# Kernel optimization log

Measured on AMD Instinct MI355X. Metric: run time of the kernel, lower is better.

## Reference

```python
import jax, jax.numpy as jnp
import numpy as np


def setup_inputs() -> dict:
    key = jax.random.key(0)
    k1, k2, k3 = jax.random.split(key, 3)
    B, T1, T2, D, MP = 16, 256, 256, 256, 32
    reps_lt = jax.random.normal(k1, (B, T1, D), dtype=jnp.float32)
    reps_rt = jax.random.normal(k2, (B, T2, D), dtype=jnp.float32)
    # keras 'uniform' initializer ~ U(-0.05, 0.05); stored as [mp, d]
    kernel = jax.random.uniform(k3, (MP, D), dtype=jnp.float32, minval=-0.05, maxval=0.05)
    return {"reps_lt": reps_lt, "reps_rt": reps_rt, "kernel": kernel}


def reference(reps_lt, reps_rt, kernel):
    # reps_lt: [b, t1, d], reps_rt: [b, t2, d], kernel: [mp, d]
    # Original: broadcast lt*kernel -> [b,t1,1,mp,d], rt -> [b,1,t2,1,d],
    # cosine_norm=False => tanh(sum over d), then max over t1.
    lt_m = reps_lt[:, :, None, :] * kernel[None, None, :, :]      # [b, t1, mp, d]
    scores = jnp.einsum('bimd,bjd->bijm', lt_m, reps_rt)           # [b, t1, t2, mp]
    match = jnp.tanh(scores)
    return jnp.max(match, axis=1)                                  # [b, t2, mp]
```

## Files before the change

### kernel.cpp

```cpp
#include <hip/hip_runtime.h>
#include <hip/hip_bf16.h>
#include <math.h>

#define Bn   16
#define T1n  256
#define T2n  256
#define Dn   256
#define MPn  32

typedef __attribute__((ext_vector_type(8))) short short8;
typedef __attribute__((ext_vector_type(4))) float f32x4;

typedef const __attribute__((address_space(1))) void* gp_t;
typedef __attribute__((address_space(3))) void* lp_t;

__device__ __forceinline__ void gl_lds16(const void* g, void* l) {
  __builtin_amdgcn_global_load_lds((gp_t)g, (lp_t)l, 16, 0, 0);
}

__device__ inline short f2b(float f) {
  __hip_bfloat16 h = __float2bfloat16(f);
  return __builtin_bit_cast(short, h);
}
__device__ inline float b2f(short s) {
  unsigned int u = ((unsigned int)(unsigned short)s) << 16;
  return __builtin_bit_cast(float, u);
}
__device__ inline float max4(f32x4 a) {
  return fmaxf(fmaxf(a.x, a.y), fmaxf(a.z, a.w));
}

__device__ inline int swz_chunk(int row, int d8) {
  return row * 32 + (d8 ^ (row & 7));
}

__global__ __launch_bounds__(256, 8)
void cvt_bf16_kernel(const float* __restrict__ lt, const float* __restrict__ rt,
                     short* __restrict__ olt, short* __restrict__ ort) {
  int blk = blockIdx.x;
  const float* src;
  short* dst;
  int t;
  if (blk < 512) { src = lt; dst = olt; t = blk * 256 + threadIdx.x; }
  else           { src = rt; dst = ort; t = (blk - 512) * 256 + threadIdx.x; }
  const f32x4* s = reinterpret_cast<const f32x4*>(src + (size_t)t * 8);
  f32x4 f0 = s[0], f1 = s[1];
  short8 v;
  v[0] = f2b(f0.x); v[1] = f2b(f0.y); v[2] = f2b(f0.z); v[3] = f2b(f0.w);
  v[4] = f2b(f1.x); v[5] = f2b(f1.y); v[6] = f2b(f1.z); v[7] = f2b(f1.w);
  *reinterpret_cast<short8*>(dst + (size_t)t * 8) = v;
}

__global__ __launch_bounds__(256, 3)
void mp_match_kernel(const short* __restrict__ ltb,
                     const short* __restrict__ rtb,
                     const float* __restrict__ kern,
                     float* __restrict__ out) {
  __shared__ short lds_rt[32 * 256];
  __shared__ short lds_lt[2][32 * 256];

  const int bid = blockIdx.x;
  const int xcd = bid & 7;
  const int idx = bid >> 3;
  const int b   = ((idx >> 6) << 3) | xcd;
  const int rem = idx & 63;
  const int jblk = rem & 7;
  const int mg   = rem >> 3;
  const int j0   = jblk * 32;

  const int tid  = threadIdx.x;
  const int lane = tid & 63;
  const int w    = tid >> 6;
  const int m    = mg * 4 + w;
  const int bl   = lane & 15;
  const int hl   = lane >> 4;

  int soff[4];
  #pragma unroll
  for (int it = 0; it < 4; ++it) {
    int cidx = it * 256 + tid;
    int row = cidx >> 5, slot = cidx & 31;
    soff[it] = row * 256 + (slot ^ (row & 7)) * 8;
  }
  const int wub = (tid & ~63) * 8;

  const short* rbase = rtb + ((size_t)b * T2n + j0) * Dn;
  #pragma unroll
  for (int it = 0; it < 4; ++it)
    gl_lds16(rbase + soff[it], &lds_rt[it * 256 * 8 + wub]);
  asm volatile("s_waitcnt vmcnt(0)" ::: "memory");
  __syncthreads();

  const short* lbase = ltb + (size_t)b * T1n * Dn;
  #pragma unroll
  for (int it = 0; it < 4; ++it)
    gl_lds16(lbase + soff[it], &lds_lt[0][it * 256 * 8 + wub]);

  short8 bsc[2][8];
  {
    const float* kbase = kern + (size_t)m * Dn;
    #pragma unroll
    for (int kk = 0; kk < 8; ++kk) {
      int d8 = kk * 4 + hl;
      const f32x4* kp = reinterpret_cast<const f32x4*>(kbase + d8 * 8);
      f32x4 k0 = kp[0], k1 = kp[1];
      #pragma unroll
      for (int sub = 0; sub < 2; ++sub) {
        int brow = sub * 16 + bl;
        short8 r = *reinterpret_cast<const short8*>(&lds_rt[swz_chunk(brow, d8) * 8]);
        short8 v;
        v[0] = f2b(b2f(r[0]) * k0.x); v[1] = f2b(b2f(r[1]) * k0.y);
        v[2] = f2b(b2f(r[2]) * k0.z); v[3] = f2b(b2f(r[3]) * k0.w);
        v[4] = f2b(b2f(r[4]) * k1.x); v[5] = f2b(b2f(r[5]) * k1.y);
        v[6] = f2b(b2f(r[6]) * k1.z); v[7] = f2b(b2f(r[7]) * k1.w);
        bsc[sub][kk] = v;
      }
    }
  }

  float jmax0 = -1e30f, jmax1 = -1e30f;

  asm volatile("s_waitcnt vmcnt(0)" ::: "memory");
  __syncthreads();

  for (int ic = 0; ic < 8; ++ic) {
    const int cur = ic & 1;
    if (ic < 7) {
      #pragma unroll
      for (int it = 0; it < 4; ++it)
        gl_lds16(lbase + (ic + 1) * 32 * 256 + soff[it],
                 &lds_lt[cur ^ 1][it * 256 * 8 + wub]);
    }
    const short* lcur = lds_lt[cur];
    f32x4 a00 = {0.f,0.f,0.f,0.f}, a01 = {0.f,0.f,0.f,0.f};
    f32x4 a10 = {0.f,0.f,0.f,0.f}, a11 = {0.f,0.f,0.f,0.f};
    #pragma unroll
    for (int kk = 0; kk < 8; ++kk) {
      int d8 = kk * 4 + hl;
      short8 A0 = *reinterpret_cast<const short8*>(&lcur[swz_chunk(bl, d8) * 8]);
      short8 A1 = *reinterpret_cast<const short8*>(&lcur[swz_chunk(16 + bl, d8) * 8]);
      a00 = __builtin_amdgcn_mfma_f32_16x16x32_bf16(A0, bsc[0][kk], a00, 0, 0, 0);
      a01 = __builtin_amdgcn_mfma_f32_16x16x32_bf16(A0, bsc[1][kk], a01, 0, 0, 0);
      a10 = __builtin_amdgcn_mfma_f32_16x16x32_bf16(A1, bsc[0][kk], a10, 0, 0, 0);
      a11 = __builtin_amdgcn_mfma_f32_16x16x32_bf16(A1, bsc[1][kk], a11, 0, 0, 0);
    }
    jmax0 = fmaxf(jmax0, fmaxf(max4(a00), max4(a10)));
    jmax1 = fmaxf(jmax1, fmaxf(max4(a01), max4(a11)));
    if (ic < 7) {
      asm volatile("s_waitcnt vmcnt(0)" ::: "memory");
      __syncthreads();
    }
  }

  jmax0 = fmaxf(jmax0, __shfl_xor(jmax0, 16));
  jmax0 = fmaxf(jmax0, __shfl_xor(jmax0, 32));
  jmax1 = fmaxf(jmax1, __shfl_xor(jmax1, 16));
  jmax1 = fmaxf(jmax1, __shfl_xor(jmax1, 32));
  if (hl < 2) {
    float v = hl ? jmax1 : jmax0;
    int j = j0 + hl * 16 + bl;
    out[((size_t)b * T2n + j) * MPn + m] = tanhf(v);
  }
}

extern "C" void kernel_launch(void* const* d_in, const int* in_sizes, int n_in,
                              void* d_out, int out_size, void* d_ws, size_t ws_size,
                              hipStream_t stream) {
  const float* lt   = (const float*)d_in[0];
  const float* rt   = (const float*)d_in[1];
  const float* kern = (const float*)d_in[2];
  float* out = (float*)d_out;

  short* ltb = (short*)d_ws;
  short* rtb = ltb + (size_t)Bn * T1n * Dn;

  cvt_bf16_kernel<<<1024, 256, 0, stream>>>(lt, rt, ltb, rtb);
  mp_match_kernel<<<1024, 256, 0, stream>>>(ltb, rtb, kern, out);
}
```

Before: 28.68 us.

## Drop LDS staging and read bf16 operands directly from global memory

Removes the shared-memory double buffer and async global-to-LDS copies. Each wave now loads its MFMA A and B fragments straight from global memory, relying on L2/L1 caching since the four waves of a block read the same lt rows. The inner loop becomes 16 chunks of 16 rows with two MFMAs per step, and occupancy is raised to 4 blocks per SIMD. This removes block-wide barriers and LDS traffic, but exposes global load latency with no explicit prefetch and makes each wave issue redundant global loads.

```diff
diff --git a/kernel.cpp b/kernel.cpp
--- a/kernel.cpp
+++ b/kernel.cpp
@@ -11,13 +11,6 @@
 typedef __attribute__((ext_vector_type(8))) short short8;
 typedef __attribute__((ext_vector_type(4))) float f32x4;
 
-typedef const __attribute__((address_space(1))) void* gp_t;
-typedef __attribute__((address_space(3))) void* lp_t;
-
-__device__ __forceinline__ void gl_lds16(const void* g, void* l) {
-  __builtin_amdgcn_global_load_lds((gp_t)g, (lp_t)l, 16, 0, 0);
-}
-
 __device__ inline short f2b(float f) {
   __hip_bfloat16 h = __float2bfloat16(f);
   return __builtin_bit_cast(short, h);
@@ -28,10 +21,6 @@
 }
 __device__ inline float max4(f32x4 a) {
   return fmaxf(fmaxf(a.x, a.y), fmaxf(a.z, a.w));
-}
-
-__device__ inline int swz_chunk(int row, int d8) {
-  return row * 32 + (d8 ^ (row & 7));
 }
 
 __global__ __launch_bounds__(256, 8)
@@ -51,14 +40,11 @@
   *reinterpret_cast<short8*>(dst + (size_t)t * 8) = v;
 }
 
-__global__ __launch_bounds__(256, 3)
+__global__ __launch_bounds__(256, 4)
 void mp_match_kernel(const short* __restrict__ ltb,
                      const short* __restrict__ rtb,
                      const float* __restrict__ kern,
                      float* __restrict__ out) {
-  __shared__ short lds_rt[32 * 256];
-  __shared__ short lds_lt[2][32 * 256];
-
   const int bid = blockIdx.x;
   const int xcd = bid & 7;
   const int idx = bid >> 3;
@@ -75,81 +61,44 @@
   const int bl   = lane & 15;
   const int hl   = lane >> 4;
 
-  int soff[4];
-  #pragma unroll
-  for (int it = 0; it < 4; ++it) {
-    int cidx = it * 256 + tid;
-    int row = cidx >> 5, slot = cidx & 31;
-    soff[it] = row * 256 + (slot ^ (row & 7)) * 8;
-  }
-  const int wub = (tid & ~63) * 8;
+  const short* ltbase = ltb + (size_t)b * T1n * Dn;
+  const short* rtbase = rtb + ((size_t)b * T2n + j0) * Dn;
+  const float* kbase  = kern + (size_t)m * Dn;
 
-  const short* rbase = rtb + ((size_t)b * T2n + j0) * Dn;
-  #pragma unroll
-  for (int it = 0; it < 4; ++it)
-    gl_lds16(rbase + soff[it], &lds_rt[it * 256 * 8 + wub]);
-  asm volatile("s_waitcnt vmcnt(0)" ::: "memory");
-  __syncthreads();
-
-  const short* lbase = ltb + (size_t)b * T1n * Dn;
-  #pragma unroll
-  for (int it = 0; it < 4; ++it)
-    gl_lds16(lbase + soff[it], &lds_lt[0][it * 256 * 8 + wub]);
+  const int foff = bl * Dn + hl * 8;
 
   short8 bsc[2][8];
-  {
-    const float* kbase = kern + (size_t)m * Dn;
+  #pragma unroll
+  for (int kk = 0; kk < 8; ++kk) {
+    const f32x4* kp = reinterpret_cast<const f32x4*>(kbase + (kk * 4 + hl) * 8);
+    f32x4 k0 = kp[0], k1 = kp[1];
     #pragma unroll
-    for (int kk = 0; kk < 8; ++kk) {
-      int d8 = kk * 4 + hl;
-      const f32x4* kp = reinterpret_cast<const f32x4*>(kbase + d8 * 8);
-      f32x4 k0 = kp[0], k1 = kp[1];
-      #pragma unroll
-      for (int sub = 0; sub < 2; ++sub) {
-        int brow = sub * 16 + bl;
-        short8 r = *reinterpret_cast<const short8*>(&lds_rt[swz_chunk(brow, d8) * 8]);
-        short8 v;
-        v[0] = f2b(b2f(r[0]) * k0.x); v[1] = f2b(b2f(r[1]) * k0.y);
-        v[2] = f2b(b2f(r[2]) * k0.z); v[3] = f2b(b2f(r[3]) * k0.w);
-        v[4] = f2b(b2f(r[4]) * k1.x); v[5] = f2b(b2f(r[5]) * k1.y);
-        v[6] = f2b(b2f(r[6]) * k1.z); v[7] = f2b(b2f(r[7]) * k1.w);
-        bsc[sub][kk] = v;
-      }
+    for (int sub = 0; sub < 2; ++sub) {
+      short8 r = *reinterpret_cast<const short8*>(rtbase + sub * 16 * Dn + foff + kk * 32);
+      short8 v;
+      v[0] = f2b(b2f(r[0]) * k0.x); v[1] = f2b(b2f(r[1]) * k0.y);
+      v[2] = f2b(b2f(r[2]) * k0.z); v[3] = f2b(b2f(r[3]) * k0.w);
+      v[4] = f2b(b2f(r[4]) * k1.x); v[5] = f2b(b2f(r[5]) * k1.y);
+      v[6] = f2b(b2f(r[6]) * k1.z); v[7] = f2b(b2f(r[7]) * k1.w);
+      bsc[sub][kk] = v;
     }
   }
 
   float jmax0 = -1e30f, jmax1 = -1e30f;
 
-  asm volatile("s_waitcnt vmcnt(0)" ::: "memory");
-  __syncthreads();
-
-  for (int ic = 0; ic < 8; ++ic) {
-    const int cur = ic & 1;
-    if (ic < 7) {
-      #pragma unroll
-      for (int it = 0; it < 4; ++it)
-        gl_lds16(lbase + (ic + 1) * 32 * 256 + soff[it],
-                 &lds_lt[cur ^ 1][it * 256 * 8 + wub]);
-    }
-    const short* lcur = lds_lt[cur];
-    f32x4 a00 = {0.f,0.f,0.f,0.f}, a01 = {0.f,0.f,0.f,0.f};
-    f32x4 a10 = {0.f,0.f,0.f,0.f}, a11 = {0.f,0.f,0.f,0.f};
+  #pragma unroll 1
+  for (int ic = 0; ic < 16; ++ic) {
+    const short* abase = ltbase + ic * 16 * Dn + foff;
+    f32x4 a0 = {0.f, 0.f, 0.f, 0.f};
+    f32x4 a1 = {0.f, 0.f, 0.f, 0.f};
     #pragma unroll
     for (int kk = 0; kk < 8; ++kk) {
-      int d8 = kk * 4 + hl;
-      short8 A0 = *reinterpret_cast<const short8*>(&lcur[swz_chunk(bl, d8) * 8]);
-      short8 A1 = *reinterpret_cast<const short8*>(&lcur[swz_chunk(16 + bl, d8) * 8]);
-      a00 = __builtin_amdgcn_mfma_f32_16x16x32_bf16(A0, bsc[0][kk], a00, 0, 0, 0);
-      a01 = __builtin_amdgcn_mfma_f32_16x16x32_bf16(A0, bsc[1][kk], a01, 0, 0, 0);
-      a10 = __builtin_amdgcn_mfma_f32_16x16x32_bf16(A1, bsc[0][kk], a10, 0, 0, 0);
-      a11 = __builtin_amdgcn_mfma_f32_16x16x32_bf16(A1, bsc[1][kk], a11, 0, 0, 0);
+      short8 A = *reinterpret_cast<const short8*>(abase + kk * 32);
+      a0 = __builtin_amdgcn_mfma_f32_16x16x32_bf16(A, bsc[0][kk], a0, 0, 0, 0);
+      a1 = __builtin_amdgcn_mfma_f32_16x16x32_bf16(A, bsc[1][kk], a1, 0, 0, 0);
     }
-    jmax0 = fmaxf(jmax0, fmaxf(max4(a00), max4(a10)));
-    jmax1 = fmaxf(jmax1, fmaxf(max4(a01), max4(a11)));
-    if (ic < 7) {
-      asm volatile("s_waitcnt vmcnt(0)" ::: "memory");
-      __syncthreads();
-    }
+    jmax0 = fmaxf(jmax0, max4(a0));
+    jmax1 = fmaxf(jmax1, max4(a1));
   }
 
   jmax0 = fmaxf(jmax0, __shfl_xor(jmax0, 16));
```

Result: slower. 75.98 us (+164.9%).

## Widen j tile to 64 rows, prefetch two lt stages, halve grid

Applied to the files above, without the earlier changes.

Each block now covers 64 rt rows instead of 32, so every lt tile loaded from LDS feeds four MFMA column blocks. This halves the grid and the total lt global traffic. The lt pipeline is restructured to issue the first two stages up front, refill the just-consumed buffer after a barrier, and use partial vmcnt waits. It also raises wave priority around the MFMA loop. The cost is more registers (bsc grows to 4x8 short8) and lower occupancy (launch bounds 2), and only 512 blocks run on 256 CUs.

```diff
diff --git a/kernel.cpp b/kernel.cpp
--- a/kernel.cpp
+++ b/kernel.cpp
@@ -17,6 +17,13 @@
 __device__ __forceinline__ void gl_lds16(const void* g, void* l) {
   __builtin_amdgcn_global_load_lds((gp_t)g, (lp_t)l, 16, 0, 0);
 }
+__device__ __forceinline__ void fence() { asm volatile("" ::: "memory"); }
+__device__ __forceinline__ void bar() {
+  fence();
+  __builtin_amdgcn_s_barrier();
+  fence();
+}
+#define WAIT_VM(N) asm volatile("s_waitcnt vmcnt(" #N ")" ::: "memory")
 
 __device__ inline short f2b(float f) {
   __hip_bfloat16 h = __float2bfloat16(f);
@@ -51,22 +58,22 @@
   *reinterpret_cast<short8*>(dst + (size_t)t * 8) = v;
 }
 
-__global__ __launch_bounds__(256, 3)
+__global__ __launch_bounds__(256, 2)
 void mp_match_kernel(const short* __restrict__ ltb,
                      const short* __restrict__ rtb,
                      const float* __restrict__ kern,
                      float* __restrict__ out) {
-  __shared__ short lds_rt[32 * 256];
+  __shared__ short lds_rt[64 * 256];
   __shared__ short lds_lt[2][32 * 256];
 
   const int bid = blockIdx.x;
   const int xcd = bid & 7;
   const int idx = bid >> 3;
-  const int b   = ((idx >> 6) << 3) | xcd;
-  const int rem = idx & 63;
-  const int jblk = rem & 7;
-  const int mg   = rem >> 3;
-  const int j0   = jblk * 32;
+  const int b   = ((idx >> 5) << 3) | xcd;
+  const int rem = idx & 31;
+  const int jblk = rem & 3;
+  const int mg   = rem >> 2;
+  const int j0   = jblk * 64;
 
   const int tid  = threadIdx.x;
   const int lane = tid & 63;
@@ -75,80 +82,107 @@
   const int bl   = lane & 15;
   const int hl   = lane >> 4;
 
-  int soff[4];
+  const short* lbase = ltb + (size_t)b * T1n * Dn;
+  const short* rbase = rtb + ((size_t)b * T2n + j0) * Dn;
+  const float* kbase = kern + (size_t)m * Dn;
+
+  int soffL[4];
   #pragma unroll
   for (int it = 0; it < 4; ++it) {
     int cidx = it * 256 + tid;
     int row = cidx >> 5, slot = cidx & 31;
-    soff[it] = row * 256 + (slot ^ (row & 7)) * 8;
+    soffL[it] = row * 256 + (slot ^ (row & 7)) * 8;
   }
   const int wub = (tid & ~63) * 8;
 
-  const short* rbase = rtb + ((size_t)b * T2n + j0) * Dn;
+  f32x4 kq[8][2];
+  #pragma unroll
+  for (int kk = 0; kk < 8; ++kk) {
+    const f32x4* kp = reinterpret_cast<const f32x4*>(kbase + (kk * 4 + hl) * 8);
+    kq[kk][0] = kp[0];
+    kq[kk][1] = kp[1];
+  }
+  fence();
+  #pragma unroll
+  for (int it = 0; it < 8; ++it) {
+    int cidx = it * 256 + tid;
+    int row = cidx >> 5, slot = cidx & 31;
+    gl_lds16(rbase + row * 256 + (slot ^ (row & 7)) * 8,
+             &lds_rt[it * 256 * 8 + wub]);
+  }
+  fence();
   #pragma unroll
   for (int it = 0; it < 4; ++it)
-    gl_lds16(rbase + soff[it], &lds_rt[it * 256 * 8 + wub]);
-  asm volatile("s_waitcnt vmcnt(0)" ::: "memory");
-  __syncthreads();
-
-  const short* lbase = ltb + (size_t)b * T1n * Dn;
+    gl_lds16(lbase + soffL[it], &lds_lt[0][it * 256 * 8 + wub]);
+  fence();
   #pragma unroll
   for (int it = 0; it < 4; ++it)
-    gl_lds16(lbase + soff[it], &lds_lt[0][it * 256 * 8 + wub]);
-
-  short8 bsc[2][8];
-  {
-    const float* kbase = kern + (size_t)m * Dn;
+    gl_lds16(lbase + 32 * 256 + soffL[it], &lds_lt[1][it * 256 * 8 + wub]);
+  fence();
+
+  WAIT_VM(8);
+  bar();
+
+  short8 bsc[4][8];
+  #pragma unroll
+  for (int kk = 0; kk < 8; ++kk) {
+    f32x4 k0 = kq[kk][0], k1 = kq[kk][1];
     #pragma unroll
-    for (int kk = 0; kk < 8; ++kk) {
-      int d8 = kk * 4 + hl;
-      const f32x4* kp = reinterpret_cast<const f32x4*>(kbase + d8 * 8);
-      f32x4 k0 = kp[0], k1 = kp[1];
-      #pragma unroll
-      for (int sub = 0; sub < 2; ++sub) {
-        int brow = sub * 16 + bl;
-        short8 r = *reinterpret_cast<const short8*>(&lds_rt[swz_chunk(brow, d8) * 8]);
-        short8 v;
-        v[0] = f2b(b2f(r[0]) * k0.x); v[1] = f2b(b2f(r[1]) * k0.y);
-        v[2] = f2b(b2f(r[2]) * k0.z); v[3] = f2b(b2f(r[3]) * k0.w);
-        v[4] = f2b(b2f(r[4]) * k1.x); v[5] = f2b(b2f(r[5]) * k1.y);
-        v[6] = f2b(b2f(r[6]) * k1.z); v[7] = f2b(b2f(r[7]) * k1.w);
-        bsc[sub][kk] = v;
-      }
+    for (int sub = 0; sub < 4; ++sub) {
+      int brow = sub * 16 + bl;
+      short8 r = *reinterpret_cast<const short8*>(
+          &lds_rt[swz_chunk(brow, kk * 4 + hl) * 8]);
+      short8 v;
+      v[0] = f2b(b2f(r[0]) * k0.x); v[1] = f2b(b2f(r[1]) * k0.y);
+      v[2] = f2b(b2f(r[2]) * k0.z); v[3] = f2b(b2f(r[3]) * k0.w);
+      v[4] = f2b(b2f(r[4]) * k1.x); v[5] = f2b(b2f(r[5]) * k1.y);
+      v[6] = f2b(b2f(r[6]) * k1.z); v[7] = f2b(b2f(r[7]) * k1.w);
+      bsc[sub][kk] = v;
     }
   }
 
-  float jmax0 = -1e30f, jmax1 = -1e30f;
-
-  asm volatile("s_waitcnt vmcnt(0)" ::: "memory");
-  __syncthreads();
-
+  WAIT_VM(4);
+  bar();
+
+  float jmax0 = -1e30f, jmax1 = -1e30f, jmax2 = -1e30f, jmax3 = -1e30f;
+
+  #pragma unroll 1
   for (int ic = 0; ic < 8; ++ic) {
     const int cur = ic & 1;
-    if (ic < 7) {
+    const short* lcur = lds_lt[cur];
+    __builtin_amdgcn_s_setprio(1);
+    #pragma unroll
+    for (int it2 = 0; it2 < 2; ++it2) {
+      int arow = it2 * 16 + bl;
+      f32x4 a0 = {0.f,0.f,0.f,0.f}, a1 = {0.f,0.f,0.f,0.f};
+      f32x4 a2 = {0.f,0.f,0.f,0.f}, a3 = {0.f,0.f,0.f,0.f};
+      #pragma unroll
+      for (int kk = 0; kk < 8; ++kk) {
+        short8 A = *reinterpret_cast<const short8*>(
+            &lcur[swz_chunk(arow, kk * 4 + hl) * 8]);
+        a0 = __builtin_amdgcn_mfma_f32_16x16x32_bf16(A, bsc[0][kk], a0, 0, 0, 0);
+        a1 = __builtin_amdgcn_mfma_f32_16x16x32_bf16(A, bsc[1][kk], a1, 0, 0, 0);
+        a2 = __builtin_amdgcn_mfma_f32_16x16x32_bf16(A, bsc[2][kk], a2, 0, 0, 0);
+        a3 = __builtin_amdgcn_mfma_f32_16x16x32_bf16(A, bsc[3][kk], a3, 0, 0, 0);
+      }
+      jmax0 = fmaxf(jmax0, max4(a0));
+      jmax1 = fmaxf(jmax1, max4(a1));
+      jmax2 = fmaxf(jmax2, max4(a2));
+      jmax3 = fmaxf(jmax3, max4(a3));
+    }
+    __builtin_amdgcn_s_setprio(0);
+    bar();
+    if (ic < 6) {
       #pragma unroll
       for (int it = 0; it < 4; ++it)
-        gl_lds16(lbase + (ic + 1) * 32 * 256 + soff[it],
-                 &lds_lt[cur ^ 1][it * 256 * 8 + wub]);
-    }
-    const short* lcur = lds_lt[cur];
-    f32x4 a00 = {0.f,0.f,0.f,0.f}, a01 = {0.f,0.f,0.f,0.f};
-    f32x4 a10 = {0.f,0.f,0.f,0.f}, a11 = {0.f,0.f,0.f,0.f};
-    #pragma unroll
-    for (int kk = 0; kk < 8; ++kk) {
-      int d8 = kk * 4 + hl;
-      short8 A0 = *reinterpret_cast<const short8*>(&lcur[swz_chunk(bl, d8) * 8]);
-      short8 A1 = *reinterpret_cast<const short8*>(&lcur[swz_chunk(16 + bl, d8) * 8]);
-      a00 = __builtin_amdgcn_mfma_f32_16x16x32_bf16(A0, bsc[0][kk], a00, 0, 0, 0);
-      a01 = __builtin_amdgcn_mfma_f32_16x16x32_bf16(A0, bsc[1][kk], a01, 0, 0, 0);
-      a10 = __builtin_amdgcn_mfma_f32_16x16x32_bf16(A1, bsc[0][kk], a10, 0, 0, 0);
-      a11 = __builtin_amdgcn_mfma_f32_16x16x32_bf16(A1, bsc[1][kk], a11, 0, 0, 0);
-    }
-    jmax0 = fmaxf(jmax0, fmaxf(max4(a00), max4(a10)));
-    jmax1 = fmaxf(jmax1, fmaxf(max4(a01), max4(a11)));
-    if (ic < 7) {
-      asm volatile("s_waitcnt vmcnt(0)" ::: "memory");
-      __syncthreads();
+        gl_lds16(lbase + (ic + 2) * 32 * 256 + soffL[it],
+                 &lds_lt[cur][it * 256 * 8 + wub]);
+      fence();
+      WAIT_VM(4);
+      bar();
+    } else if (ic == 6) {
+      WAIT_VM(0);
+      bar();
     }
   }
 
@@ -156,11 +190,13 @@
   jmax0 = fmaxf(jmax0, __shfl_xor(jmax0, 32));
   jmax1 = fmaxf(jmax1, __shfl_xor(jmax1, 16));
   jmax1 = fmaxf(jmax1, __shfl_xor(jmax1, 32));
-  if (hl < 2) {
-    float v = hl ? jmax1 : jmax0;
-    int j = j0 + hl * 16 + bl;
-    out[((size_t)b * T2n + j) * MPn + m] = tanhf(v);
-  }
+  jmax2 = fmaxf(jmax2, __shfl_xor(jmax2, 16));
+  jmax2 = fmaxf(jmax2, __shfl_xor(jmax2, 32));
+  jmax3 = fmaxf(jmax3, __shfl_xor(jmax3, 16));
+  jmax3 = fmaxf(jmax3, __shfl_xor(jmax3, 32));
+  float v = (hl == 0) ? jmax0 : (hl == 1) ? jmax1 : (hl == 2) ? jmax2 : jmax3;
+  int j = j0 + hl * 16 + bl;
+  out[((size_t)b * T2n + j) * MPn + m] = tanhf(v);
 }
 
 extern "C" void kernel_launch(void* const* d_in, const int* in_sizes, int n_in,
@@ -175,5 +211,5 @@
   short* rtb = ltb + (size_t)Bn * T1n * Dn;
 
   cvt_bf16_kernel<<<1024, 256, 0, stream>>>(lt, rt, ltb, rtb);
-  mp_match_kernel<<<1024, 256, 0, stream>>>(ltb, rtb, kern, out);
-}
+  mp_match_kernel<<<512, 256, 0, stream>>>(ltb, rtb, kern, out);
+}
```

Result: faster. 27.21 us (-5.1%).
